# Kernel optimization log

Hardware: AMD Instinct MI355X
Metric: run time of the kernel (lower is better)

Reference implementation:

```python
import jax, jax.numpy as jnp
import numpy as np

H = 12      # num_heads
EPS = 1e-5  # LayerNorm eps (torch default)


def _ln(x, g, b):
    m = x.mean(-1, keepdims=True)
    v = x.var(-1, keepdims=True)
    return (x - m) * jax.lax.rsqrt(v + EPS) * g + b


def _rot_half(x):
    x1, x2 = x[..., 0::2], x[..., 1::2]
    return jnp.stack((-x2, x1), axis=-1).reshape(x.shape)


def _rope_tables(n, head_dim):
    # rotary-embedding-torch: RotaryEmbedding(dim=head_dim//2, use_xpos=True),
    # theta=10000, scale_base=512. Only first rot=head_dim//2 dims are rotated.
    rot = head_dim // 2
    inv = 1.0 / (10000.0 ** (jnp.arange(0, rot, 2, dtype=jnp.float32) / rot))
    t = jnp.arange(n, dtype=jnp.float32)
    freqs = jnp.repeat(t[:, None] * inv[None, :], 2, axis=-1)  # (n, rot), interleaved
    base = (jnp.arange(0, rot, 2, dtype=jnp.float32) + 0.4 * rot) / (1.4 * rot)
    power = (t - n // 2) / 512.0
    sc = base[None, :] ** power[:, None]
    sc = jnp.concatenate([sc, sc], axis=-1)  # (n, rot), concatenated (library behavior)
    return jnp.cos(freqs), jnp.sin(freqs), sc


def _attn_path(xn, Wqkv, bqkv, Wproj, bproj, qg, qb, kg, kb, R, rg, rb):
    B, N, D = xn.shape
    d = D // H
    qkv = xn @ Wqkv + bqkv
    q, k, v = jnp.split(qkv, 3, axis=-1)
    hd = lambda t: t.reshape(B, N, H, d).transpose(0, 2, 1, 3)  # (B,H,N,d)
    q, k, v = hd(q), hd(k), hd(v)
    q = _ln(q, qg, qb)  # per-head QK LayerNorm
    k = _ln(k, kg, kb)
    cos, sin, sc = _rope_tables(N, d)
    rot = d // 2

    def rope(t, s):  # rotate only first rot dims
        tl, tr = t[..., :rot], t[..., rot:]
        tl = tl * cos * s + _rot_half(tl) * sin * s
        return jnp.concatenate([tl, tr], axis=-1)

    q = rope(q, sc)
    v = rope(v, 1.0 / sc)  # source applies rope to (q, v), not k

    scores = jnp.einsum('bhid,bhjd->bhij', q, k) / jnp.sqrt(jnp.asarray(d, xn.dtype))
    p = jax.nn.softmax(scores, axis=-1)
    # SDPA(q,k,ones_NN)[...,i,j] == sum_k p[...,i,k] for every j (constant over j).
    # All downstream ops (head-mix einsum, LayerNorm over heads, @ v) therefore
    # reduce exactly to the per-(b,i) computation below, avoiding an N^3 matmul.
    s = p.sum(-1)                              # (B,H,N)
    mix = jnp.einsum('bhi,hg->big', s, R)      # (B,N,H)
    w = _ln(mix, rg, rb)                       # reattn LayerNorm over head axis
    vsum = v.sum(axis=2)                       # (B,H,d); (w @ v) with w const over j
    y = jnp.einsum('big,bgd->bigd', w, vsum).reshape(B, N, D)
    return y @ Wproj + bproj


def _cgmlp(xn, W1, b1, gg, gb, cw, cb, W2, b2):
    h = jax.nn.gelu(xn @ W1 + b1, approximate=False)
    c2 = h.shape[-1] // 2
    xr, xg = h[..., :c2], h[..., c2:]
    xg = _ln(xg, gg, gb).transpose(0, 2, 1)  # (B,C,T)
    K = cw.shape[-1]
    xg = jax.lax.conv_general_dilated(xg, cw, (1,), [((K - 1) // 2, (K - 1) // 2)],
                                      dimension_numbers=('NCH', 'OIH', 'NCH'),
                                      feature_group_count=c2)  # depthwise conv1d
    xg = (xg + cb[None, :, None]).transpose(0, 2, 1)
    return (xr * xg) @ W2 + b2


def reference(x, Wqkv, bqkv, Wproj, bproj, qn_g, qn_b, kn_g, kn_b, reattn_w, rn_g, rn_b,
              ln1_g, ln1_b, ln2_g, ln2_b, ls1, ls2, W1, b1, gn_g, gn_b, conv_w, conv_b,
              W2, b2, Wout, bout):
    # eval mode: dropout / drop_path are identity
    xa = _ln(x, ln1_g, ln1_b)
    attn = sum(_attn_path(xa, Wqkv[p], bqkv[p], Wproj[p], bproj[p], qn_g[p], qn_b[p],
                          kn_g[p], kn_b[p], reattn_w[p], rn_g[p], rn_b[p])
               for p in range(2))
    x_attn = x + ls1 * attn
    xm = _ln(x, ln2_g, ln2_b)
    x_mlp = x + ls2 * _cgmlp(xm, W1, b1, gn_g, gn_b, conv_w, conv_b, W2, b2)
    xf = jnp.concatenate([x_attn, x_mlp], axis=-1)
    return xf @ Wout + bout + x


def setup_inputs():
    B, N, D, P = 4, 1024, 768, 2
    d = D // H
    C = 4 * D
    c2 = C // 2
    K = 21
    ks = iter(jax.random.split(jax.random.key(0), 16))
    nrm = lambda s, sd=0.02: jax.random.normal(next(ks), s, jnp.float32) * sd
    return {
        'x': jax.random.normal(next(ks), (B, N, D), jnp.float32),
        'Wqkv': nrm((P, D, 3 * D)), 'bqkv': jnp.zeros((P, 3 * D)),
        'Wproj': nrm((P, D, D)), 'bproj': jnp.zeros((P, D)),
        'qn_g': jnp.ones((P, d)), 'qn_b': jnp.zeros((P, d)),
        'kn_g': jnp.ones((P, d)), 'kn_b': jnp.zeros((P, d)),
        'reattn_w': jax.random.normal(next(ks), (P, H, H), jnp.float32),
        'rn_g': jnp.ones((P, H)), 'rn_b': jnp.zeros((P, H)),
        'ln1_g': jnp.ones((D,)), 'ln1_b': jnp.zeros((D,)),
        'ln2_g': jnp.ones((D,)), 'ln2_b': jnp.zeros((D,)),
        'ls1': jnp.full((D,), 0.01, jnp.float32), 'ls2': jnp.full((D,), 0.01, jnp.float32),
        'W1': nrm((D, C)), 'b1': jnp.zeros((C,)),
        'gn_g': jnp.ones((c2,)), 'gn_b': jnp.zeros((c2,)),
        'conv_w': nrm((c2, 1, K), 0.1), 'conv_b': jnp.zeros((c2,)),
        'W2': nrm((c2, D)), 'b2': jnp.zeros((D,)),
        'Wout': nrm((2 * D, D)), 'bout': jnp.zeros((D,)),
    }
```

## Files before the change

### kernel.cpp

```cpp
#include <hip/hip_runtime.h>
#include <hip/hip_bf16.h>

typedef short s16x8 __attribute__((ext_vector_type(8)));
typedef float f32x4 __attribute__((ext_vector_type(4)));

#define C2 1536

__device__ __forceinline__ float b2f(ushort u){ return __uint_as_float(((unsigned)u)<<16); }
__device__ __forceinline__ ushort f2b(float f){ unsigned u = __float_as_uint(f); return (ushort)((u + 0x7fffu + ((u>>16)&1u)) >> 16); }

#define GL16(g, l) __builtin_amdgcn_global_load_lds( \
    (const __attribute__((address_space(1))) void*)(g), \
    (__attribute__((address_space(3))) void*)(l), 16, 0, 0)

#define VMW(n) asm volatile("s_waitcnt vmcnt(" #n ")" ::: "memory")
#define LGW()  asm volatile("s_waitcnt lgkmcnt(0)" ::: "memory")
#define SB()   __builtin_amdgcn_sched_barrier(0)
#define BAR()  __builtin_amdgcn_s_barrier()
#define SP1    __builtin_amdgcn_s_setprio(1)
#define SP0    __builtin_amdgcn_s_setprio(0)
#define MF(va, vb, c) __builtin_amdgcn_mfma_f32_16x16x32_bf16(va, vb, c, 0,0,0)

#define RDA(P, mh) { const int ab = (P) + aro + (mh)*4096; \
    a0=L8(ab+sx0);      a1=L8(ab+sx1); \
    a2=L8(ab+1024+sx0); a3=L8(ab+1024+sx1); \
    a4=L8(ab+2048+sx0); a5=L8(ab+2048+sx1); \
    a6=L8(ab+3072+sx0); a7=L8(ab+3072+sx1); }
#define RDB0(P, nh) { const int bb = (P) + bro + (nh)*2048; \
    b00=L8(bb+sx0); b01=L8(bb+sx1); b02=L8(bb+1024+sx0); b03=L8(bb+1024+sx1); }
#define RDB1(P, nh) { const int bb = (P) + bro + (nh)*2048; \
    b10=L8(bb+sx0); b11=L8(bb+sx1); b12=L8(bb+1024+sx0); b13=L8(bb+1024+sx1); }
#define L8(off) (*(const s16x8*)&lds[off])
#define STG(p0, p1, T, dstb) { \
    GL16((p0) + (size_t)(T)*64, &lds[(dstb) + ldsw]); \
    GL16((p1) + (size_t)(T)*64, &lds[(dstb) + 4096 + ldsw]); }
#define QD(mh, nh, B0,B1,B2,B3) { \
  acc[(mh)*4+0][(nh)*2+0]=MF(a0,B0,acc[(mh)*4+0][(nh)*2+0]); \
  acc[(mh)*4+0][(nh)*2+0]=MF(a1,B1,acc[(mh)*4+0][(nh)*2+0]); \
  acc[(mh)*4+0][(nh)*2+1]=MF(a0,B2,acc[(mh)*4+0][(nh)*2+1]); \
  acc[(mh)*4+0][(nh)*2+1]=MF(a1,B3,acc[(mh)*4+0][(nh)*2+1]); \
  acc[(mh)*4+1][(nh)*2+0]=MF(a2,B0,acc[(mh)*4+1][(nh)*2+0]); \
  acc[(mh)*4+1][(nh)*2+0]=MF(a3,B1,acc[(mh)*4+1][(nh)*2+0]); \
  acc[(mh)*4+1][(nh)*2+1]=MF(a2,B2,acc[(mh)*4+1][(nh)*2+1]); \
  acc[(mh)*4+1][(nh)*2+1]=MF(a3,B3,acc[(mh)*4+1][(nh)*2+1]); \
  acc[(mh)*4+2][(nh)*2+0]=MF(a4,B0,acc[(mh)*4+2][(nh)*2+0]); \
  acc[(mh)*4+2][(nh)*2+0]=MF(a5,B1,acc[(mh)*4+2][(nh)*2+0]); \
  acc[(mh)*4+2][(nh)*2+1]=MF(a4,B2,acc[(mh)*4+2][(nh)*2+1]); \
  acc[(mh)*4+2][(nh)*2+1]=MF(a5,B3,acc[(mh)*4+2][(nh)*2+1]); \
  acc[(mh)*4+3][(nh)*2+0]=MF(a6,B0,acc[(mh)*4+3][(nh)*2+0]); \
  acc[(mh)*4+3][(nh)*2+0]=MF(a7,B1,acc[(mh)*4+3][(nh)*2+0]); \
  acc[(mh)*4+3][(nh)*2+1]=MF(a6,B2,acc[(mh)*4+3][(nh)*2+1]); \
  acc[(mh)*4+3][(nh)*2+1]=MF(a7,B3,acc[(mh)*4+3][(nh)*2+1]); }

#define EIGHT(t0, t1, DS, VM4) \
   VMW(4); BAR(); \
  RDA(0,0); RDB0(0,0); \
  STG(pA00,pA01,(t1), 16384); \
  LGW(); SB(); SP1; QD(0,0,b00,b01,b02,b03); SP0; BAR(); \
   RDB1(0,1); \
  STG(pA10,pA11,(t1), 24576); \
  BAR(); LGW(); SB(); SP1; QD(0,1,b10,b11,b12,b13); SP0; BAR(); \
   RDA(0,1); \
  if (DS) { STG(pB00,pB01,(t0)+2, 32768); } \
  BAR(); LGW(); SB(); SP1; QD(1,0,b00,b01,b02,b03); SP0; BAR(); \
   if (DS) { STG(pB10,pB11,(t0)+2, 40960); } \
  BAR(); SP1; QD(1,1,b10,b11,b12,b13); SP0; BAR(); \
   VM4; BAR(); \
  RDA(16384,0); RDB0(16384,0); \
  if (DS) { STG(pA00,pA01,(t0)+2, 0); } \
  LGW(); SB(); SP1; QD(0,0,b00,b01,b02,b03); SP0; BAR(); \
   RDB1(16384,1); \
  if (DS) { STG(pA10,pA11,(t0)+2, 8192); } \
  BAR(); LGW(); SB(); SP1; QD(0,1,b10,b11,b12,b13); SP0; BAR(); \
   RDA(16384,1); \
  if (DS) { STG(pB00,pB01,(t1)+2, 49152); } \
  BAR(); LGW(); SB(); SP1; QD(1,0,b00,b01,b02,b03); SP0; BAR(); \
   if (DS) { STG(pB10,pB11,(t1)+2, 57344); } \
  BAR(); SP1; QD(1,1,b10,b11,b12,b13); SP0; BAR();

template<int EPI>
__global__ __launch_bounds__(512, 1) void gemm256(
    const ushort* __restrict__ A, const ushort* __restrict__ BT,
    int M, int N, int K,
    const float* __restrict__ bias,
    ushort* __restrict__ o16, ushort* __restrict__ o16b)
{
    extern __shared__ ushort lds[];
    const int t = threadIdx.x;
    const int lane = t & 63, wv = t >> 6;
    const int wr = wv >> 2, wc = wv & 3;
    const int r0 = lane & 15, q = lane >> 4, e7 = lane & 7;
    const int m0 = blockIdx.y*256, n0 = blockIdx.x*256;

    const int idx = wv*64 + lane;
    const int lr8 = idx >> 3;
    const int ksrc = (idx & 7) ^ (lr8 & 7);
    const ushort* pA00 = A  + (size_t)(m0 +   0 +  0 + lr8)*K + ksrc*8;
    const ushort* pA01 = A  + (size_t)(m0 +   0 + 64 + lr8)*K + ksrc*8;
    const ushort* pA10 = A  + (size_t)(m0 + 128 +  0 + lr8)*K + ksrc*8;
    const ushort* pA11 = A  + (size_t)(m0 + 128 + 64 + lr8)*K + ksrc*8;
    const ushort* pB00 = BT + (size_t)(n0 +   0 +  0 + lr8)*K + ksrc*8;
    const ushort* pB01 = BT + (size_t)(n0 +   0 + 64 + lr8)*K + ksrc*8;
    const ushort* pB10 = BT + (size_t)(n0 + 128 +  0 + lr8)*K + ksrc*8;
    const ushort* pB11 = BT + (size_t)(n0 + 128 + 64 + lr8)*K + ksrc*8;
    const int ldsw = wv*512;

    const int aro = (wr*128 + r0)*64;
    const int bro = 32768 + (wc*64 + r0)*64;
    const int sx0 = (q ^ e7)*8, sx1 = ((q ^ e7)*8) ^ 32;

    f32x4 acc[8][4];
    #pragma unroll
    for (int i=0;i<8;++i)
        #pragma unroll
        for (int j=0;j<4;++j) acc[i][j] = (f32x4){0.f,0.f,0.f,0.f};
    s16x8 a0,a1,a2,a3,a4,a5,a6,a7;
    s16x8 b00,b01,b02,b03, b10,b11,b12,b13;

    const int nkt = K >> 6;
    const int niter = nkt >> 1;

    STG(pB00,pB01, 0, 32768);
    STG(pB10,pB11, 0, 40960);
    STG(pA00,pA01, 0, 0);
    STG(pA10,pA11, 0, 8192);
    STG(pB00,pB01, 1, 49152);
    STG(pB10,pB11, 1, 57344);

    for (int i = 0; i < niter-1; ++i) {
        const int t0 = 2*i, t1 = 2*i+1;
        EIGHT(t0, t1, 1, VMW(4));
    }
    {
        const int t0 = nkt-2, t1 = nkt-1;
        EIGHT(t0, t1, 0, VMW(0));
    }

    #pragma unroll
    for (int gm=0; gm<8; ++gm) {
        #pragma unroll
        for (int gn=0; gn<4; ++gn) {
            int col = n0 + wc*64 + gn*16 + r0;
            #pragma unroll
            for (int r=0; r<4; ++r) {
                int row = m0 + wr*128 + gm*16 + q*4 + r;
                float v = acc[gm][gn][r];
                if (EPI == 0) {
                    o16[(size_t)row*N + col] = f2b(v + bias[col]);
                } else {
                    v += bias[col];
                    float g = 0.5f*v*(1.0f + erff(v*0.70710678118f));
                    if (col < C2) o16 [(size_t)row*C2 + col]        = f2b(g);
                    else          o16b[(size_t)row*C2 + (col - C2)] = f2b(g);
                }
            }
        }
    }
}

template<int EPI>
__global__ __launch_bounds__(256) void gemm_bf16(
    const ushort* __restrict__ A, const ushort* __restrict__ BT,
    int M, int N, int K, int lda, int ldbt,
    const float* __restrict__ bias, const float* __restrict__ xres,
    ushort* __restrict__ o16, float* __restrict__ o32)
{
    __shared__ ushort Al[2][128*32];
    __shared__ ushort Bl[2][128*32];
    const int t = threadIdx.x;
    const int m0 = blockIdx.y*128, n0 = blockIdx.x*128;
    const int lane = t & 63, wv = t >> 6;
    const int wm = (wv>>1)*64, wn = (wv&1)*64;
    const int r0 = lane & 15, q = lane >> 4;

    const int c0i = t, c1i = t + 256;
    const int lrow0 = ((c0i>>6)<<4) | (c0i&15), lkc0 = ((c0i>>4)&3) << 3;
    const int lrow1 = ((c1i>>6)<<4) | (c1i&15), lkc1 = ((c1i>>4)&3) << 3;
    const ushort* gA0 = A  + (size_t)(m0+lrow0)*lda + lkc0;
    const ushort* gB0 = BT + (size_t)(n0+lrow0)*ldbt + lkc0;
    const ushort* gA1 = A  + (size_t)(m0+lrow1)*lda + lkc1;
    const ushort* gB1 = BT + (size_t)(n0+lrow1)*ldbt + lkc1;

    f32x4 acc[4][4];
    #pragma unroll
    for (int i=0;i<4;++i)
        #pragma unroll
        for (int j=0;j<4;++j) acc[i][j] = (f32x4){0.f,0.f,0.f,0.f};

    const int nkt = K >> 5;
    uint4 pa0_0, pb0_0, pa1_0, pb1_0;
    uint4 pa0_1, pb0_1, pa1_1, pb1_1;
    pa0_0 = *(const uint4*)gA0;        pb0_0 = *(const uint4*)gB0;
    pa1_0 = *(const uint4*)gA1;        pb1_0 = *(const uint4*)gB1;
    pa0_1 = *(const uint4*)(gA0 + 32); pb0_1 = *(const uint4*)(gB0 + 32);
    pa1_1 = *(const uint4*)(gA1 + 32); pb1_1 = *(const uint4*)(gB1 + 32);
    *(uint4*)&Al[0][c0i*8] = pa0_0;
    *(uint4*)&Bl[0][c0i*8] = pb0_0;
    *(uint4*)&Al[0][c1i*8] = pa1_0;
    *(uint4*)&Bl[0][c1i*8] = pb1_0;

    for (int kt = 0; kt < nkt; kt += 2) {
        __syncthreads();
        {
            s16x8 af[4], bfr[4];
            #pragma unroll
            for (int mt=0; mt<4; ++mt) af[mt]  = *(const s16x8*)&Al[0][(((wm>>4)+mt)*64 + lane)*8];
            #pragma unroll
            for (int nt=0; nt<4; ++nt) bfr[nt] = *(const s16x8*)&Bl[0][(((wn>>4)+nt)*64 + lane)*8];
            *(uint4*)&Al[1][c0i*8] = pa0_1;
            *(uint4*)&Bl[1][c0i*8] = pb0_1;
            *(uint4*)&Al[1][c1i*8] = pa1_1;
            *(uint4*)&Bl[1][c1i*8] = pb1_1;
            if (kt+2 < nkt) {
                pa0_0 = *(const uint4*)(gA0 + (kt+2)*32);
                pb0_0 = *(const uint4*)(gB0 + (kt+2)*32);
                pa1_0 = *(const uint4*)(gA1 + (kt+2)*32);
                pb1_0 = *(const uint4*)(gB1 + (kt+2)*32);
            }
            #pragma unroll
            for (int mt=0; mt<4; ++mt)
                #pragma unroll
                for (int nt=0; nt<4; ++nt)
                    acc[mt][nt] = __builtin_amdgcn_mfma_f32_16x16x32_bf16(af[mt], bfr[nt], acc[mt][nt], 0,0,0);
        }
        __syncthreads();
        {
            s16x8 af[4], bfr[4];
            #pragma unroll
            for (int mt=0; mt<4; ++mt) af[mt]  = *(const s16x8*)&Al[1][(((wm>>4)+mt)*64 + lane)*8];
            #pragma unroll
            for (int nt=0; nt<4; ++nt) bfr[nt] = *(const s16x8*)&Bl[1][(((wn>>4)+nt)*64 + lane)*8];
            if (kt+2 < nkt) {
                *(uint4*)&Al[0][c0i*8] = pa0_0;
                *(uint4*)&Bl[0][c0i*8] = pb0_0;
                *(uint4*)&Al[0][c1i*8] = pa1_0;
                *(uint4*)&Bl[0][c1i*8] = pb1_0;
            }
            if (kt+3 < nkt) {
                pa0_1 = *(const uint4*)(gA0 + (kt+3)*32);
                pb0_1 = *(const uint4*)(gB0 + (kt+3)*32);
                pa1_1 = *(const uint4*)(gA1 + (kt+3)*32);
                pb1_1 = *(const uint4*)(gB1 + (kt+3)*32);
            }
            #pragma unroll
            for (int mt=0; mt<4; ++mt)
                #pragma unroll
                for (int nt=0; nt<4; ++nt)
                    acc[mt][nt] = __builtin_amdgcn_mfma_f32_16x16x32_bf16(af[mt], bfr[nt], acc[mt][nt], 0,0,0);
        }
    }

    #pragma unroll
    for (int mt=0; mt<4; ++mt) {
        #pragma unroll
        for (int nt=0; nt<4; ++nt) {
            int col = n0 + wn + nt*16 + r0;
            #pragma unroll
            for (int r=0; r<4; ++r) {
                int row = m0 + wm + mt*16 + q*4 + r;
                float v = acc[mt][nt][r];
                if (EPI == 0) {
                    o16[(size_t)row*N + col] = f2b(v + bias[col]);
                } else if (EPI == 3) {
                    o32[(size_t)row*768 + col] = v + bias[(row>>10)*768 + col] + xres[(size_t)row*768 + col];
                } else {
                    o16[(size_t)row*2304 + 768 + col] = f2b(v);
                }
            }
        }
    }
}

__global__ __launch_bounds__(256) void mega_prep(
    const float* __restrict__ Wqkv, const float* __restrict__ W1,
    const float* __restrict__ Wout, const float* __restrict__ W2,
    const float* __restrict__ ls2,  const float* __restrict__ bqkv,
    const float* __restrict__ x,
    const float* __restrict__ g1, const float* __restrict__ b1v,
    const float* __restrict__ g2, const float* __restrict__ b2v,
    const float* __restrict__ R,  const float* __restrict__ rng,
    const float* __restrict__ rnb, const float* __restrict__ bproj,
    const float* __restrict__ bout,
    ushort* __restrict__ WvT, ushort* __restrict__ W1T, ushort* __restrict__ BTf,
    ushort* __restrict__ Afold, ushort* __restrict__ BT2, float* __restrict__ bvp,
    float* __restrict__ w1t, float* __restrict__ w2t, float* __restrict__ wvec,
    float* __restrict__ attn_c, float* __restrict__ vsum, float* __restrict__ cvecb,
    ushort* __restrict__ xa, ushort* __restrict__ xm, ushort* __restrict__ xc)
{
    __shared__ float tl[32*33];
    const int blk = blockIdx.x;
    const int t = threadIdx.x;

    if (blk < 1152) {
        int p = blk / 576, l = blk % 576;
        int kt = (l % 24)*32, nt = (l / 24)*32;
        const float* src = Wqkv + (size_t)p*768*2304;
        ushort* dst = WvT + (size_t)p*768*768;
        int nl = t & 31, kg = t >> 5;
        #pragma unroll
        for (int kk=0; kk<4; ++kk) {
            int k = kg*4 + kk;
            tl[k*33 + nl] = src[(size_t)(kt + k)*2304 + 1536 + nt + nl];
        }
        __syncthreads();
        int kcol = t & 31, ng = t >> 5;
        #pragma unroll
        for (int nn=0; nn<4; ++nn) {
            int nrow = ng*4 + nn;
            dst[(size_t)(nt + nrow)*768 + kt + kcol] = f2b(tl[kcol*33 + nrow]);
        }
    } else if (blk < 3456) {
        int l = blk - 1152;
        int kt = (l % 24)*32, nt = (l / 24)*32;
        int nl = t & 31, kg = t >> 5;
        #pragma unroll
        for (int kk=0; kk<4; ++kk) {
            int k = kg*4 + kk;
            tl[k*33 + nl] = W1[(size_t)(kt + k)*3072 + nt + nl];
        }
        __syncthreads();
        int kcol = t & 31, ng = t >> 5;
        #pragma unroll
        for (int nn=0; nn<4; ++nn) {
            int nrow = ng*4 + nn;
            W1T[(size_t)(nt + nrow)*768 + kt + kcol] = f2b(tl[kcol*33 + nrow]);
        }
    } else if (blk < 4032) {
        int l = blk - 3456;
        int kt = (l % 24)*32, nt = (l / 24)*32;
        int nl = t & 31, kg = t >> 5;
        #pragma unroll
        for (int kk=0; kk<4; ++kk) {
            int k = kg*4 + kk;
            tl[k*33 + nl] = Wout[(size_t)(kt + k)*768 + nt + nl]
                          + Wout[(size_t)(768 + kt + k)*768 + nt + nl];
        }
        __syncthreads();
        int kcol = t & 31, ng = t >> 5;
        #pragma unroll
        for (int nn=0; nn<4; ++nn) {
            int nrow = ng*4 + nn;
            BTf[(size_t)(nt + nrow)*2304 + kt + kcol] = f2b(tl[kcol*33 + nrow]);
        }
    } else if (blk < 4608) {
        int l = blk - 4032;
        int kt = (l % 24)*32, nt = (l / 24)*32;
        const float* src = Wout + (size_t)768*768;
        int nl = t & 31, kg = t >> 5;
        #pragma unroll
        for (int kk=0; kk<4; ++kk) {
            int k = kg*4 + kk;
            tl[k*33 + nl] = src[(size_t)(kt + k)*768 + nt + nl];
        }
        __syncthreads();
        int kcol = t & 31, ng = t >> 5;
        #pragma unroll
        for (int nn=0; nn<4; ++nn) {
            int nrow = ng*4 + nn;
            Afold[(size_t)(nt + nrow)*768 + kt + kcol] = f2b(tl[kcol*33 + nrow] * ls2[kt + kcol]);
        }
    } else if (blk < 9216) {
        int i = (blk - 4608)*256 + t;
        BT2[i] = f2b(W2[i]);
    } else if (blk < 9222) {
        int i = (blk - 9216)*256 + t;
        if (i < 1536) bvp[i] = bqkv[(i/768)*2304 + 1536 + (i%768)];
    } else if (blk < 9478) {
        int pb = blk - 9222;
        int idx = pb*256 + t;
        {
            int i = idx >> 6, j = idx & 63;
            float w1, w2;
            if (j < 32) {
                int m = j >> 1;
                float inv = powf(10000.f, -(float)m*(1.f/16.f));
                float fr = (float)i * inv;
                float c = cosf(fr), sn = sinf(fr);
                float power = ((float)i - 512.f) * (1.f/512.f);
                float basev = (2.f*(float)(j & 15) + 12.8f) * (1.f/44.8f);
                float sfac = powf(basev, -power);
                w1 = c * sfac;
                w2 = ((j & 1) ? sn : -sn) * sfac;
            } else { w1 = 1.f; w2 = 0.f; }
            w1t[idx] = w1; w2t[idx] = w2;
        }
        if (pb >= 1 && pb <= 12) {
            int k = (pb-1)*256 + t;
            int o = k % 768;
            attn_c[k] = bproj[o] + bproj[768 + o];
        }
        if (pb >= 13 && pb <= 36) {
            int k = (pb-13)*256 + t;
            vsum[k] = 0.f;
        }
        if (pb >= 37 && pb <= 48) {
            int k = (pb-37)*256 + t;
            cvecb[k] = bout[k % 768];
        }
        if (pb == 0) {
            float* mixs = tl;
            float* wsb  = tl + 32;
            if (t < 24) {
                int p = t / 12, g = t % 12;
                float m = 0.f;
                for (int h=0; h<12; ++h) m += R[p*144 + h*12 + g];
                mixs[t] = m;
            }
            __syncthreads();
            if (t < 2) {
                float mean=0.f, var=0.f;
                for (int g=0; g<12; ++g) mean += mixs[t*12+g];
                mean *= (1.f/12.f);
                for (int g=0; g<12; ++g){ float d = mixs[t*12+g]-mean; var += d*d; }
                var *= (1.f/12.f);
                float rstd = rsqrtf(var + 1e-5f);
                for (int g=0; g<12; ++g)
                    wsb[t*12+g] = (mixs[t*12+g]-mean)*rstd*rng[t*12+g] + rnb[t*12+g];
            }
            __syncthreads();
            if (t < 24) wvec[t] = wsb[t];
        }
    } else {
        int row = blk - 9478;
        float* sb = tl;
        float v[3]; float s = 0.f, ss = 0.f;
        #pragma unroll
        for (int e=0; e<3; ++e) { v[e] = x[(size_t)row*768 + t + e*256]; s += v[e]; ss += v[e]*v[e]; }
        for (int o=32; o>0; o>>=1){ s += __shfl_down(s,o,64); ss += __shfl_down(ss,o,64); }
        int lane = t&63, w = t>>6;
        if (lane==0){ sb[w]=s; sb[4+w]=ss; }
        __syncthreads();
        s = sb[0]+sb[1]+sb[2]+sb[3]; ss = sb[4]+sb[5]+sb[6]+sb[7];
        float mean = s*(1.f/768.f);
        float var  = ss*(1.f/768.f) - mean*mean;
        float rstd = rsqrtf(var + 1e-5f);
        #pragma unroll
        for (int e=0; e<3; ++e){
            int c = t + e*256;
            float n = (v[e]-mean)*rstd;
            xa[(size_t)row*768 + c] = f2b(n*g1[c] + b1v[c]);
            xm[(size_t)row*768 + c] = f2b(n*g2[c] + b2v[c]);
            xc[(size_t)row*2304 + c] = f2b(v[e]);
        }
    }
}

__global__ __launch_bounds__(256) void rope_reduce(const ushort* __restrict__ V,
    const float* __restrict__ w1t, const float* __restrict__ w2t, float* __restrict__ vsum)
{
    int col = blockIdx.x*256 + threadIdx.x;
    int b = blockIdx.y;
    int i0 = blockIdx.z * 64;
    int j = col & 63;
    float acc = 0.f;
    const ushort* vp = V + (size_t)(b*1024 + i0)*1536;
    #pragma unroll 4
    for (int i=0; i<64; ++i) {
        float v1 = b2f(vp[(size_t)i*1536 + col]);
        float v2 = b2f(vp[(size_t)i*1536 + (col^1)]);
        int ii = i0 + i;
        acc += w1t[ii*64 + j]*v1 + w2t[ii*64 + j]*v2;
    }
    atomicAdd(&vsum[b*1536 + col], acc);
}

__global__ __launch_bounds__(256) void attn_gemm(const float* __restrict__ vsum,
    const float* __restrict__ wvec, const float* __restrict__ Wproj, float* __restrict__ attn_c)
{
    int o  = blockIdx.x*256 + threadIdx.x;
    int c0 = blockIdx.y * 96;
    int b  = blockIdx.z;
    int p  = c0 / 768;
    float acc = 0.f;
    #pragma unroll 4
    for (int cc=0; cc<96; ++cc) {
        int c = c0 + cc;
        int cl = c - p*768;
        float y = wvec[p*12 + (cl>>6)] * vsum[b*1536 + c];
        acc += y * Wproj[(size_t)p*589824 + (size_t)cl*768 + o];
    }
    atomicAdd(&attn_c[b*768 + o], acc);
}

__global__ __launch_bounds__(256) void cvec_kernel(const float* __restrict__ attn_c,
    const float* __restrict__ ls1, const float* __restrict__ ls2, const float* __restrict__ b2,
    const float* __restrict__ Wout, float* __restrict__ cvecb)
{
    int o  = blockIdx.x*256 + threadIdx.x;
    int r0 = blockIdx.y * 96;
    int b  = blockIdx.z;
    float acc = 0.f;
    #pragma unroll 4
    for (int rr = 0; rr < 96; ++rr) {
        int r = r0 + rr;
        float coef = (r < 768) ? ls1[r]*attn_c[b*768 + r]
                               : ls2[r-768]*b2[r-768];
        acc += coef * Wout[(size_t)r*768 + o];
    }
    atomicAdd(&cvecb[b*768 + o], acc);
}

__global__ __launch_bounds__(256) void ln_gate(const ushort* __restrict__ xg,
    const float* __restrict__ g, const float* __restrict__ bta, ushort* __restrict__ out)
{
    __shared__ float sb[8];
    int row = blockIdx.x, t = threadIdx.x;
    float v[6]; float s=0.f, ss=0.f;
    #pragma unroll
    for (int e=0;e<6;++e){ v[e] = b2f(xg[(size_t)row*1536 + t + e*256]); s+=v[e]; ss+=v[e]*v[e]; }
    for (int o=32; o>0; o>>=1){ s += __shfl_down(s,o,64); ss += __shfl_down(ss,o,64); }
    int lane = t&63, w = t>>6;
    if (lane==0){ sb[w]=s; sb[4+w]=ss; }
    __syncthreads();
    s = sb[0]+sb[1]+sb[2]+sb[3]; ss = sb[4]+sb[5]+sb[6]+sb[7];
    float mean = s*(1.f/1536.f);
    float var  = ss*(1.f/1536.f) - mean*mean;
    float rstd = rsqrtf(var + 1e-5f);
    #pragma unroll
    for (int e=0;e<6;++e){
        int c = t + e*256;
        out[(size_t)row*1536 + c] = f2b((v[e]-mean)*rstd*g[c] + bta[c]);
    }
}

#define CROWS 128
#define CIN   (CROWS + 20)
#define CSTR  72
__global__ __launch_bounds__(256) void conv_mul(const ushort* __restrict__ xgln,
    const float* __restrict__ cw, const float* __restrict__ cb,
    const ushort* __restrict__ xr, ushort* __restrict__ u)
{
    __shared__ ushort tile[CIN * CSTR];
    const int c0 = blockIdx.x * 64;
    const int i0 = blockIdx.y * CROWS;
    const int b  = blockIdx.z;
    const int t  = threadIdx.x;
    const size_t base = (size_t)b*1024*1536;

    #pragma unroll
    for (int it = 0; it < 5; ++it) {
        int idx = it*256 + t;
        if (idx < CIN*8) {
            int r  = idx >> 3;
            int cq = (idx & 7) * 8;
            int si = i0 + r - 10;
            uint4 val = make_uint4(0u,0u,0u,0u);
            if (si >= 0 && si < 1024)
                val = *(const uint4*)(xgln + base + (size_t)si*1536 + c0 + cq);
            *(uint4*)&tile[r*CSTR + cq] = val;
        }
    }
    __syncthreads();

    const int ch = t & 63;
    const int o0 = (t >> 6) * 32;
    const int c  = c0 + ch;

    float w[21];
    #pragma unroll
    for (int k=0; k<21; ++k) w[k] = cw[c*21 + k];
    const float bias = cb[c];

    float win[21];
    #pragma unroll
    for (int j=0; j<20; ++j) win[j] = b2f(tile[(o0+j)*CSTR + ch]);

    #pragma unroll
    for (int j=0; j<32; ++j) {
        win[(j+20)%21] = b2f(tile[(o0+j+20)*CSTR + ch]);
        float acc = bias;
        #pragma unroll
        for (int k=0; k<21; ++k) acc += win[(j+k)%21] * w[k];
        size_t offr = base + (size_t)(i0+o0+j)*1536 + c;
        u[(size_t)(b*1024 + i0+o0+j)*2304 + 768 + c] = f2b(b2f(xr[offr]) * acc);
    }
}

extern "C" void kernel_launch(void* const* d_in, const int* in_sizes, int n_in,
                              void* d_out, int out_size, void* d_ws, size_t ws_size,
                              hipStream_t stream)
{
    const float* x     = (const float*)d_in[0];
    const float* Wqkv  = (const float*)d_in[1];
    const float* bqkv  = (const float*)d_in[2];
    const float* Wproj = (const float*)d_in[3];
    const float* bproj = (const float*)d_in[4];
    const float* Rw    = (const float*)d_in[9];
    const float* rng   = (const float*)d_in[10];
    const float* rnb   = (const float*)d_in[11];
    const float* ln1g  = (const float*)d_in[12];
    const float* ln1b  = (const float*)d_in[13];
    const float* ln2g  = (const float*)d_in[14];
    const float* ln2b  = (const float*)d_in[15];
    const float* ls1   = (const float*)d_in[16];
    const float* ls2   = (const float*)d_in[17];
    const float* W1    = (const float*)d_in[18];
    const float* b1    = (const float*)d_in[19];
    const float* gng   = (const float*)d_in[20];
    const float* gnb   = (const float*)d_in[21];
    const float* cw    = (const float*)d_in[22];
    const float* cb    = (const float*)d_in[23];
    const float* W2    = (const float*)d_in[24];
    const float* b2    = (const float*)d_in[25];
    const float* Wout  = (const float*)d_in[26];
    const float* bout  = (const float*)d_in[27];
    float* out = (float*)d_out;

    char* ws = (char*)d_ws;
    size_t off = 0;
    auto alloc = [&](size_t bytes)->char* {
        char* p = ws + off;
        off += (bytes + 255) & ~(size_t)255;
        return p;
    };
    ushort* WvT   = (ushort*)alloc(1536*768*2);
    ushort* W1T   = (ushort*)alloc(3072*768*2);
    ushort* BT2   = (ushort*)alloc(1536*768*2);
    ushort* Afold = (ushort*)alloc(768*768*2);
    ushort* BTf   = (ushort*)alloc(768*2304*2);
    float*  bvp   = (float*)alloc(1536*4);
    float*  w1t   = (float*)alloc(65536*4);
    float*  w2t   = (float*)alloc(65536*4);
    float*  wvec  = (float*)alloc(24*4);
    float*  attnc = (float*)alloc(3072*4);
    float*  vsum  = (float*)alloc(6144*4);
    float*  cvecb = (float*)alloc(3072*4);
    ushort* xa16  = (ushort*)alloc(4096*768*2);
    ushort* xm16  = (ushort*)alloc(4096*768*2);
    ushort* V16   = (ushort*)alloc(4096*1536*2);
    ushort* xg16  = (ushort*)alloc(4096*1536*2);
    ushort* xcat  = (ushort*)alloc((size_t)4096*2304*2);
    ushort* xgln  = xa16;
    ushort* xr16  = V16;
    (void)ws_size; (void)n_in; (void)in_sizes; (void)out_size;

    (void)hipFuncSetAttribute((const void*)gemm256<1>, hipFuncAttributeMaxDynamicSharedMemorySize, 131072);

    mega_prep<<<dim3(13574), 256, 0, stream>>>(
        Wqkv, W1, Wout, W2, ls2, bqkv, x,
        ln1g, ln1b, ln2g, ln2b, Rw, rng, rnb, bproj, bout,
        WvT, W1T, BTf, Afold, BT2, bvp,
        w1t, w2t, wvec, attnc, vsum, cvecb,
        xa16, xm16, xcat);

    gemm_bf16<4><<<dim3(12, 6), 256, 0, stream>>>(Afold, BT2, 768, 1536, 768, 768, 768,
                                                  nullptr, nullptr, BTf, nullptr);

    gemm_bf16<0><<<dim3(12, 32), 256, 0, stream>>>(xa16, WvT, 4096, 1536, 768, 768, 768,
                                                   bvp, nullptr, V16, nullptr);
    rope_reduce<<<dim3(6, 4, 16), 256, 0, stream>>>(V16, w1t, w2t, vsum);
    attn_gemm<<<dim3(3, 16, 4), 256, 0, stream>>>(vsum, wvec, Wproj, attnc);
    cvec_kernel<<<dim3(3, 16, 4), 256, 0, stream>>>(attnc, ls1, ls2, b2, Wout, cvecb);

    gemm256<1><<<dim3(12, 16), 512, 131072, stream>>>(xm16, W1T, 4096, 3072, 768,
                                                      b1, xr16, xg16);
    ln_gate<<<dim3(4096), 256, 0, stream>>>(xg16, gng, gnb, xgln);
    conv_mul<<<dim3(24, 8, 4), 256, 0, stream>>>(xgln, cw, cb, xr16, xcat);

    gemm_bf16<3><<<dim3(6, 32), 256, 0, stream>>>(xcat, BTf, 4096, 768, 2304, 2304, 2304,
                                                  cvecb, x, nullptr, out);
}
```

Baseline: 333.8 us.

## Fuse rope reduction into V GEMM epilogue and LayerNorm apply into conv

The V projection GEMM now reduces its outputs directly in the epilogue, weighting them with the rope tables and using shuffles plus atomics into vsum. This removes the 12.6 MB bf16 V write and the separate rope_reduce pass. The gate LayerNorm is split so a small kernel computes only per-row mean and rstd, and the normalization is applied while loading tiles in conv_mul, which avoids writing and rereading a normalized copy. The cost is extra weight-table loads and atomics in the GEMM epilogue, plus repeated normalization of halo rows in conv.

```diff
diff --git a/kernel.cpp b/kernel.cpp
--- a/kernel.cpp
+++ b/kernel.cpp
@@ -163,6 +163,7 @@
     const ushort* __restrict__ A, const ushort* __restrict__ BT,
     int M, int N, int K, int lda, int ldbt,
     const float* __restrict__ bias, const float* __restrict__ xres,
+    const float* __restrict__ w1tp, const float* __restrict__ w2tp, float* __restrict__ vsump,
     ushort* __restrict__ o16, float* __restrict__ o32)
 {
     __shared__ ushort Al[2][128*32];
@@ -250,21 +251,51 @@
         }
     }
 
-    #pragma unroll
-    for (int mt=0; mt<4; ++mt) {
-        #pragma unroll
-        for (int nt=0; nt<4; ++nt) {
-            int col = n0 + wn + nt*16 + r0;
+    if (EPI == 0) {
+        float cs0=0.f, cs1=0.f, cs2=0.f, cs3=0.f;
+        #pragma unroll
+        for (int mt=0; mt<4; ++mt) {
             #pragma unroll
             for (int r=0; r<4; ++r) {
                 int row = m0 + wm + mt*16 + q*4 + r;
-                float v = acc[mt][nt][r];
-                if (EPI == 0) {
-                    o16[(size_t)row*N + col] = f2b(v + bias[col]);
-                } else if (EPI == 3) {
-                    o32[(size_t)row*768 + col] = v + bias[(row>>10)*768 + col] + xres[(size_t)row*768 + col];
-                } else {
-                    o16[(size_t)row*2304 + 768 + col] = f2b(v);
+                int ii = (row & 1023) << 6;
+                #pragma unroll
+                for (int nt=0; nt<4; ++nt) {
+                    int col = n0 + wn + nt*16 + r0;
+                    float vb = acc[mt][nt][r] + bias[col];
+                    float vn = __shfl_xor(vb, 1, 64);
+                    float c = w1tp[ii + (col & 63)]*vb + w2tp[ii + (col & 63)]*vn;
+                    if (nt == 0) cs0 += c; else if (nt == 1) cs1 += c;
+                    else if (nt == 2) cs2 += c; else cs3 += c;
+                }
+            }
+        }
+        cs0 += __shfl_xor(cs0, 16, 64); cs0 += __shfl_xor(cs0, 32, 64);
+        cs1 += __shfl_xor(cs1, 16, 64); cs1 += __shfl_xor(cs1, 32, 64);
+        cs2 += __shfl_xor(cs2, 16, 64); cs2 += __shfl_xor(cs2, 32, 64);
+        cs3 += __shfl_xor(cs3, 16, 64); cs3 += __shfl_xor(cs3, 32, 64);
+        if (lane < 16) {
+            int b = m0 >> 10;
+            atomicAdd(&vsump[b*1536 + n0 + wn +  0 + lane], cs0);
+            atomicAdd(&vsump[b*1536 + n0 + wn + 16 + lane], cs1);
+            atomicAdd(&vsump[b*1536 + n0 + wn + 32 + lane], cs2);
+            atomicAdd(&vsump[b*1536 + n0 + wn + 48 + lane], cs3);
+        }
+    } else {
+        #pragma unroll
+        for (int mt=0; mt<4; ++mt) {
+            #pragma unroll
+            for (int nt=0; nt<4; ++nt) {
+                int col = n0 + wn + nt*16 + r0;
+                #pragma unroll
+                for (int r=0; r<4; ++r) {
+                    int row = m0 + wm + mt*16 + q*4 + r;
+                    float v = acc[mt][nt][r];
+                    if (EPI == 3) {
+                        o32[(size_t)row*768 + col] = v + bias[(row>>10)*768 + col] + xres[(size_t)row*768 + col];
+                    } else {
+                        o16[(size_t)row*2304 + 768 + col] = f2b(v);
+                    }
                 }
             }
         }
@@ -445,25 +476,6 @@
     }
 }
 
-__global__ __launch_bounds__(256) void rope_reduce(const ushort* __restrict__ V,
-    const float* __restrict__ w1t, const float* __restrict__ w2t, float* __restrict__ vsum)
-{
-    int col = blockIdx.x*256 + threadIdx.x;
-    int b = blockIdx.y;
-    int i0 = blockIdx.z * 64;
-    int j = col & 63;
-    float acc = 0.f;
-    const ushort* vp = V + (size_t)(b*1024 + i0)*1536;
-    #pragma unroll 4
-    for (int i=0; i<64; ++i) {
-        float v1 = b2f(vp[(size_t)i*1536 + col]);
-        float v2 = b2f(vp[(size_t)i*1536 + (col^1)]);
-        int ii = i0 + i;
-        acc += w1t[ii*64 + j]*v1 + w2t[ii*64 + j]*v2;
-    }
-    atomicAdd(&vsum[b*1536 + col], acc);
-}
-
 __global__ __launch_bounds__(256) void attn_gemm(const float* __restrict__ vsum,
     const float* __restrict__ wvec, const float* __restrict__ Wproj, float* __restrict__ attn_c)
 {
@@ -500,14 +512,14 @@
     atomicAdd(&cvecb[b*768 + o], acc);
 }
 
-__global__ __launch_bounds__(256) void ln_gate(const ushort* __restrict__ xg,
-    const float* __restrict__ g, const float* __restrict__ bta, ushort* __restrict__ out)
+__global__ __launch_bounds__(256) void ln_stats(const ushort* __restrict__ xg,
+    float2* __restrict__ stats)
 {
     __shared__ float sb[8];
     int row = blockIdx.x, t = threadIdx.x;
-    float v[6]; float s=0.f, ss=0.f;
-    #pragma unroll
-    for (int e=0;e<6;++e){ v[e] = b2f(xg[(size_t)row*1536 + t + e*256]); s+=v[e]; ss+=v[e]*v[e]; }
+    float s=0.f, ss=0.f;
+    #pragma unroll
+    for (int e=0;e<6;++e){ float v = b2f(xg[(size_t)row*1536 + t + e*256]); s+=v; ss+=v*v; }
     for (int o=32; o>0; o>>=1){ s += __shfl_down(s,o,64); ss += __shfl_down(ss,o,64); }
     int lane = t&63, w = t>>6;
     if (lane==0){ sb[w]=s; sb[4+w]=ss; }
@@ -515,18 +527,15 @@
     s = sb[0]+sb[1]+sb[2]+sb[3]; ss = sb[4]+sb[5]+sb[6]+sb[7];
     float mean = s*(1.f/1536.f);
     float var  = ss*(1.f/1536.f) - mean*mean;
-    float rstd = rsqrtf(var + 1e-5f);
-    #pragma unroll
-    for (int e=0;e<6;++e){
-        int c = t + e*256;
-        out[(size_t)row*1536 + c] = f2b((v[e]-mean)*rstd*g[c] + bta[c]);
-    }
+    if (t == 0) stats[row] = make_float2(mean, rsqrtf(var + 1e-5f));
 }
 
 #define CROWS 128
 #define CIN   (CROWS + 20)
 #define CSTR  72
-__global__ __launch_bounds__(256) void conv_mul(const ushort* __restrict__ xgln,
+__global__ __launch_bounds__(256) void conv_mul(const ushort* __restrict__ xg,
+    const float2* __restrict__ stats,
+    const float* __restrict__ gg, const float* __restrict__ gb,
     const float* __restrict__ cw, const float* __restrict__ cb,
     const ushort* __restrict__ xr, ushort* __restrict__ u)
 {
@@ -545,8 +554,17 @@
             int cq = (idx & 7) * 8;
             int si = i0 + r - 10;
             uint4 val = make_uint4(0u,0u,0u,0u);
-            if (si >= 0 && si < 1024)
-                val = *(const uint4*)(xgln + base + (size_t)si*1536 + c0 + cq);
+            if (si >= 0 && si < 1024) {
+                uint4 raw = *(const uint4*)(xg + base + (size_t)si*1536 + c0 + cq);
+                float2 st = stats[b*1024 + si];
+                const ushort* rp = (const ushort*)&raw;
+                ushort* vp = (ushort*)&val;
+                #pragma unroll
+                for (int e=0; e<8; ++e) {
+                    int c = c0 + cq + e;
+                    vp[e] = f2b((b2f(rp[e]) - st.x)*st.y*gg[c] + gb[c]);
+                }
+            }
             *(uint4*)&tile[r*CSTR + cq] = val;
         }
     }
@@ -625,13 +643,12 @@
     float*  attnc = (float*)alloc(3072*4);
     float*  vsum  = (float*)alloc(6144*4);
     float*  cvecb = (float*)alloc(3072*4);
+    float2* stats = (float2*)alloc(4096*8);
     ushort* xa16  = (ushort*)alloc(4096*768*2);
     ushort* xm16  = (ushort*)alloc(4096*768*2);
-    ushort* V16   = (ushort*)alloc(4096*1536*2);
+    ushort* xr16  = (ushort*)alloc(4096*1536*2);
     ushort* xg16  = (ushort*)alloc(4096*1536*2);
     ushort* xcat  = (ushort*)alloc((size_t)4096*2304*2);
-    ushort* xgln  = xa16;
-    ushort* xr16  = V16;
     (void)ws_size; (void)n_in; (void)in_sizes; (void)out_size;
 
     (void)hipFuncSetAttribute((const void*)gemm256<1>, hipFuncAttributeMaxDynamicSharedMemorySize, 131072);
@@ -644,19 +661,21 @@
         xa16, xm16, xcat);
 
     gemm_bf16<4><<<dim3(12, 6), 256, 0, stream>>>(Afold, BT2, 768, 1536, 768, 768, 768,
-                                                  nullptr, nullptr, BTf, nullptr);
+                                                  nullptr, nullptr, nullptr, nullptr, nullptr,
+                                                  BTf, nullptr);
 
     gemm_bf16<0><<<dim3(12, 32), 256, 0, stream>>>(xa16, WvT, 4096, 1536, 768, 768, 768,
-                                                   bvp, nullptr, V16, nullptr);
-    rope_reduce<<<dim3(6, 4, 16), 256, 0, stream>>>(V16, w1t, w2t, vsum);
+                                                   bvp, nullptr, w1t, w2t, vsum,
+                                                   nullptr, nullptr);
     attn_gemm<<<dim3(3, 16, 4), 256, 0, stream>>>(vsum, wvec, Wproj, attnc);
     cvec_kernel<<<dim3(3, 16, 4), 256, 0, stream>>>(attnc, ls1, ls2, b2, Wout, cvecb);
 
     gemm256<1><<<dim3(12, 16), 512, 131072, stream>>>(xm16, W1T, 4096, 3072, 768,
                                                       b1, xr16, xg16);
-    ln_gate<<<dim3(4096), 256, 0, stream>>>(xg16, gng, gnb, xgln);
-    conv_mul<<<dim3(24, 8, 4), 256, 0, stream>>>(xgln, cw, cb, xr16, xcat);
+    ln_stats<<<dim3(4096), 256, 0, stream>>>(xg16, stats);
+    conv_mul<<<dim3(24, 8, 4), 256, 0, stream>>>(xg16, stats, gng, gnb, cw, cb, xr16, xcat);
 
     gemm_bf16<3><<<dim3(6, 32), 256, 0, stream>>>(xcat, BTf, 4096, 768, 2304, 2304, 2304,
-                                                  cvecb, x, nullptr, out);
-}
+                                                  cvecb, x, nullptr, nullptr, nullptr,
+                                                  nullptr, out);
+}
```

Result: faster. 325.3 us (-2.6%).
